# Optimization experiments

Hardware: AMD Instinct MI355X
Metric: run time of the kernel (lower is better)

Reference implementation:

```python
import jax, jax.numpy as jnp
import numpy as np

B, S, D, H = 4, 2048, 1024, 16
DH = D // H


def setup_inputs() -> dict:
    key = jax.random.key(0)
    ks = jax.random.split(key, 7)
    return {
        "Q": jax.random.normal(ks[0], (B, S, D), dtype=jnp.float32),
        "K": jax.random.normal(ks[1], (B, S, D), dtype=jnp.float32),
        "V": jax.random.normal(ks[2], (B, S, D), dtype=jnp.float32),
        "q_proj": jax.random.normal(ks[3], (D, D), dtype=jnp.float32),
        "k_proj": jax.random.normal(ks[4], (D, D), dtype=jnp.float32),
        "v_proj": jax.random.normal(ks[5], (D, D), dtype=jnp.float32),
        "output_proj": jax.random.normal(ks[6], (D, D), dtype=jnp.float32),
        "casual": 1,
    }


def reference(Q, K, V, q_proj, k_proj, v_proj, output_proj, casual):
    # projections: einsum('... a b, ... s b -> ... s a') == x @ W.T
    q = jnp.einsum('bsd,ad->bsa', Q, q_proj)
    k = jnp.einsum('bsd,ad->bsa', K, k_proj)
    v = jnp.einsum('bsd,ad->bsa', V, v_proj)
    # split heads: [B, S, H, DH]
    q = q.reshape(B, S, H, DH)
    k = k.reshape(B, S, H, DH)
    v = v.reshape(B, S, H, DH)
    # scores [B, H, Sq, Sk]
    scores = jnp.einsum('bqhd,bkhd->bhqk', q, k) / np.sqrt(DH).astype(np.float32)
    # causal mask: 0 on lower triangle, -inf above
    causal_mask = jnp.where(
        jnp.tril(jnp.ones((S, S), dtype=bool)), 0.0, -jnp.inf
    ).astype(scores.dtype)
    scores = scores + causal_mask
    attn = jax.nn.softmax(scores, axis=-1)
    # weighted values -> [B, Sq, H, DH] -> [B, Sq, D]
    out = jnp.einsum('bhqk,bkhd->bqhd', attn, v).reshape(B, S, D)
    # output projection: einsum('... a b, ... b -> ... a') == x @ W.T
    return jnp.einsum('bsd,ad->bsa', out, output_proj)
```

## Files before the change

kernel.cpp:

```cpp
#include <hip/hip_runtime.h>


typedef __attribute__((ext_vector_type(8))) _Float16 half8;
typedef __attribute__((ext_vector_type(4))) float f32x4;

#define DEVI static __device__ __forceinline__

static constexpr int cB = 4, cS = 2048, cD = 1024, cH = 16, cDH = 64;
static constexpr int cM = cB * cS;

DEVI unsigned short h2b(_Float16 h) { union { _Float16 f; unsigned short u; } x; x.f = h; return x.u; }

DEVI void async16(const void* g, void* l) {
#if defined(__HIP_DEVICE_COMPILE__)
  __builtin_amdgcn_global_load_lds((const __attribute__((address_space(1))) unsigned int*)g,
                                   (__attribute__((address_space(3))) unsigned int*)l, 16, 0, 0);
#endif
}

__global__ void split4_kernel(const float* __restrict__ Wq, const float* __restrict__ Wk,
                              const float* __restrict__ Wv, const float* __restrict__ Wo,
                              unsigned short* __restrict__ Wqh, unsigned short* __restrict__ Wql,
                              unsigned short* __restrict__ Wkh, unsigned short* __restrict__ Wkl,
                              unsigned short* __restrict__ Wvh, unsigned short* __restrict__ Woh) {
  const int w = blockIdx.x >> 10, blk = blockIdx.x & 1023;
  const float* in = (w == 0) ? Wq : (w == 1) ? Wk : (w == 2) ? Wv : Wo;
  unsigned short* hi = (w == 0) ? Wqh : (w == 1) ? Wkh : (w == 2) ? Wvh : Woh;
  unsigned short* lo = (w == 0) ? Wql : (w == 1) ? Wkl : nullptr;
  int i = (blk * 256 + (int)threadIdx.x) * 4;
  float4 v = *(const float4*)(in + i);
  _Float16 h0 = (_Float16)v.x, h1 = (_Float16)v.y, h2 = (_Float16)v.z, h3 = (_Float16)v.w;
  unsigned short th[4] = {h2b(h0), h2b(h1), h2b(h2), h2b(h3)};
  *(uint2*)(hi + i) = *(const uint2*)th;
  if (lo != nullptr) {
    unsigned short tl[4] = {h2b((_Float16)(v.x - (float)h0)), h2b((_Float16)(v.y - (float)h1)),
                            h2b((_Float16)(v.z - (float)h2)), h2b((_Float16)(v.w - (float)h3))};
    *(uint2*)(lo + i) = *(const uint2*)tl;
  }
}

__global__ __launch_bounds__(256, 3) void proj_fused(
    const float* __restrict__ Qa, const float* __restrict__ Ka, const float* __restrict__ Va,
    const unsigned short* __restrict__ Wqh, const unsigned short* __restrict__ Wql,
    const unsigned short* __restrict__ Wkh, const unsigned short* __restrict__ Wkl,
    const unsigned short* __restrict__ Wvh,
    unsigned short* __restrict__ qph, unsigned short* __restrict__ qpl,
    unsigned short* __restrict__ kph, unsigned short* __restrict__ kpl,
    unsigned short* __restrict__ vp) {
  constexpr int N = cD, K = cD;
  __shared__ float sA32[128 * 32];
  __shared__ unsigned short sBh[128 * 32];
  __shared__ unsigned short sBl[128 * 32];

  const int wid = (blockIdx.x & 7) * 192 + (blockIdx.x >> 3);
  const int job = wid >> 9;
  const int bid = wid & 511;
  const bool p3 = (job < 2);
  const float* A32p = (job == 0) ? Qa : (job == 1) ? Ka : Va;
  const unsigned short* Bh = (job == 0) ? Wqh : (job == 1) ? Wkh : Wvh;
  const unsigned short* Bl = (job == 0) ? Wql : Wkl;
  unsigned short* C0 = (job == 0) ? qph : (job == 1) ? kph : vp;
  unsigned short* C1 = (job == 0) ? qpl : kpl;

  const int tid = threadIdx.x, lane = tid & 63, wave = tid >> 6;
  const int wm = wave >> 1, wn = wave & 1;
  const int bm = bid >> 3, bn = bid & 7;
  const long r0 = (long)bm * 128, c0 = (long)bn * 128;
  const int quad = lane >> 4, cl = lane & 15;

  f32x4 acc[4][4];
#pragma unroll
  for (int mt = 0; mt < 4; ++mt)
#pragma unroll
    for (int nt = 0; nt < 4; ++nt) acc[mt][nt] = f32x4{0.f, 0.f, 0.f, 0.f};

  const int lrow8 = lane >> 3, lg8 = lane & 7;
  const int lrow16 = lane >> 2, lg4 = lane & 3;

  for (int k0 = 0; k0 < K; k0 += 32) {
    __syncthreads();
#pragma unroll
    for (int c = 0; c < 4; ++c) {
      int cc = wave * 4 + c;
      int r = cc * 8 + lrow8;
      const float* g = A32p + (r0 + r) * (long)K + k0 + ((lg8 ^ lrow8) * 4);
      async16(g, sA32 + cc * 256);
    }
#pragma unroll
    for (int c = 0; c < 2; ++c) {
      int cc = wave * 2 + c;
      int r = cc * 16 + lrow16;
      long gb = (c0 + r) * (long)K + k0 + ((lg4 ^ ((lrow16 >> 1) & 3)) * 8);
      async16(Bh + gb, sBh + cc * 512);
      if (p3) async16(Bl + gb, sBl + cc * 512);
    }
    __syncthreads();

    half8 ah[4], al[4], bh8[4], bl8[4];
#pragma unroll
    for (int mt = 0; mt < 4; ++mt) {
      int r = wm * 64 + mt * 16 + cl;
      int s0 = (quad * 2 + 0) ^ (r & 7), s1 = (quad * 2 + 1) ^ (r & 7);
      float fa[8];
      *(float4*)(fa) = *(const float4*)(sA32 + r * 32 + s0 * 4);
      *(float4*)(fa + 4) = *(const float4*)(sA32 + r * 32 + s1 * 4);
#pragma unroll
      for (int j = 0; j < 8; ++j) {
        _Float16 hh = (_Float16)fa[j];
        ah[mt][j] = hh;
        if (p3) al[mt][j] = (_Float16)(fa[j] - (float)hh);
      }
    }
#pragma unroll
    for (int nt = 0; nt < 4; ++nt) {
      int r = wn * 64 + nt * 16 + cl;
      int s = quad ^ ((r >> 1) & 3);
      bh8[nt] = *(const half8*)(sBh + r * 32 + s * 8);
      if (p3) bl8[nt] = *(const half8*)(sBl + r * 32 + s * 8);
    }
#pragma unroll
    for (int mt = 0; mt < 4; ++mt)
#pragma unroll
      for (int nt = 0; nt < 4; ++nt) {
        acc[mt][nt] = __builtin_amdgcn_mfma_f32_16x16x32_f16(ah[mt], bh8[nt], acc[mt][nt], 0, 0, 0);
        if (p3) {
          acc[mt][nt] = __builtin_amdgcn_mfma_f32_16x16x32_f16(ah[mt], bl8[nt], acc[mt][nt], 0, 0, 0);
          acc[mt][nt] = __builtin_amdgcn_mfma_f32_16x16x32_f16(al[mt], bh8[nt], acc[mt][nt], 0, 0, 0);
        }
      }
  }

#pragma unroll
  for (int mt = 0; mt < 4; ++mt)
#pragma unroll
    for (int nt = 0; nt < 4; ++nt)
#pragma unroll
      for (int i = 0; i < 4; ++i) {
        long row = r0 + wm * 64 + mt * 16 + quad * 4 + i;
        long col = c0 + wn * 64 + nt * 16 + cl;
        float v = acc[mt][nt][i];
        if (p3) {
          _Float16 hh = (_Float16)v;
          C0[row * N + col] = h2b(hh);
          C1[row * N + col] = h2b((_Float16)(v - (float)hh));
        } else {
          C0[row * N + col] = h2b((_Float16)v);
        }
      }
}

__global__ __launch_bounds__(256, 2) void gemm_out(const unsigned short* __restrict__ A16p,
                                                   const unsigned short* __restrict__ Bh,
                                                   float* __restrict__ C0, int M, int N, int K) {
  __shared__ unsigned short sA16[128 * 32];
  __shared__ unsigned short sBh[128 * 32];

  const int tid = threadIdx.x, lane = tid & 63, wave = tid >> 6;
  const int wm = wave >> 1, wn = wave & 1;
  const int nb = N >> 7;
  const int wid = ((int)blockIdx.x & 7) * 64 + ((int)blockIdx.x >> 3);
  const int bm = wid / nb, bn = wid % nb;
  const long r0 = (long)bm * 128, c0 = (long)bn * 128;
  const int quad = lane >> 4, cl = lane & 15;

  f32x4 acc[4][4];
#pragma unroll
  for (int mt = 0; mt < 4; ++mt)
#pragma unroll
    for (int nt = 0; nt < 4; ++nt) acc[mt][nt] = f32x4{0.f, 0.f, 0.f, 0.f};

  const int lrow16 = lane >> 2, lg4 = lane & 3;

  for (int k0 = 0; k0 < K; k0 += 32) {
    __syncthreads();
#pragma unroll
    for (int c = 0; c < 2; ++c) {
      int cc = wave * 2 + c;
      int r = cc * 16 + lrow16;
      long ga = (r0 + r) * (long)K + k0 + ((lg4 ^ ((lrow16 >> 1) & 3)) * 8);
      async16(A16p + ga, sA16 + cc * 512);
      long gb = (c0 + r) * (long)K + k0 + ((lg4 ^ ((lrow16 >> 1) & 3)) * 8);
      async16(Bh + gb, sBh + cc * 512);
    }
    __syncthreads();

    half8 ah[4], bh8[4];
#pragma unroll
    for (int mt = 0; mt < 4; ++mt) {
      int r = wm * 64 + mt * 16 + cl;
      int s = quad ^ ((r >> 1) & 3);
      ah[mt] = *(const half8*)(sA16 + r * 32 + s * 8);
    }
#pragma unroll
    for (int nt = 0; nt < 4; ++nt) {
      int r = wn * 64 + nt * 16 + cl;
      int s = quad ^ ((r >> 1) & 3);
      bh8[nt] = *(const half8*)(sBh + r * 32 + s * 8);
    }
#pragma unroll
    for (int mt = 0; mt < 4; ++mt)
#pragma unroll
      for (int nt = 0; nt < 4; ++nt)
        acc[mt][nt] = __builtin_amdgcn_mfma_f32_16x16x32_f16(ah[mt], bh8[nt], acc[mt][nt], 0, 0, 0);
  }

#pragma unroll
  for (int mt = 0; mt < 4; ++mt)
#pragma unroll
    for (int nt = 0; nt < 4; ++nt)
#pragma unroll
      for (int i = 0; i < 4; ++i) {
        long row = r0 + wm * 64 + mt * 16 + quad * 4 + i;
        long col = c0 + wn * 64 + nt * 16 + cl;
        C0[row * N + col] = acc[mt][nt][i];
      }
}

__global__ __launch_bounds__(256, 3) void flash_kernel(
    const unsigned short* __restrict__ qh_g, const unsigned short* __restrict__ ql_g,
    const unsigned short* __restrict__ kh_g, const unsigned short* __restrict__ kl_g,
    const unsigned short* __restrict__ vp_g, unsigned short* __restrict__ out) {
  __shared__ unsigned short sKh[64 * 64];
  __shared__ unsigned short sKl[64 * 64];
  __shared__ unsigned int sVtU[64 * 34];
  __shared__ unsigned short sP[4][32 * 40];

  const int tid = threadIdx.x, lane = tid & 63, wave = tid >> 6;
  const int quad = lane >> 4, cl = lane & 15;
  const int bh = blockIdx.x & 63;
  const int qt = 15 - (blockIdx.x >> 6);
  const int h = bh & 15;
  const int b = bh >> 4;
  const long rowbase = (long)b * cS;
  const int q0 = qt * 128;
  const int lrow8 = lane >> 3, lg8 = lane & 7;

  half8 qh[2][2], ql[2][2];
  const _Float16 s8 = (_Float16)0.125f;
#pragma unroll
  for (int ks = 0; ks < 2; ++ks)
#pragma unroll
    for (int mt = 0; mt < 2; ++mt) {
      long r = rowbase + q0 + wave * 32 + mt * 16 + cl;
      long off = r * cD + h * 64 + ks * 32 + quad * 8;
      qh[ks][mt] = *(const half8*)(qh_g + off) * s8;
      ql[ks][mt] = *(const half8*)(ql_g + off) * s8;
    }

  f32x4 O[2][5];
  float mrow[2][4];
#pragma unroll
  for (int mt = 0; mt < 2; ++mt) {
#pragma unroll
    for (int dt = 0; dt < 5; ++dt) O[mt][dt] = f32x4{0.f, 0.f, 0.f, 0.f};
#pragma unroll
    for (int i = 0; i < 4; ++i) mrow[mt][i] = -1e30f;
  }

  half8 vone;
#pragma unroll
  for (int j = 0; j < 8; ++j) vone[j] = (cl == 0) ? (_Float16)1.0f : (_Float16)0.0f;

  auto tile = [&](int ki, bool MASK) {
    __syncthreads();
#pragma unroll
    for (int c = 0; c < 2; ++c) {
      int cc = wave * 2 + c;
      int r = cc * 8 + lrow8;
      long g = (rowbase + ki * 64 + r) * (long)cD + h * 64 + ((lg8 ^ lrow8) * 8);
      async16(kh_g + g, sKh + cc * 512);
      async16(kl_g + g, sKl + cc * 512);
    }
    {
      int r2 = tid & 31, dc = (tid >> 5) * 8;
      const unsigned short* gv = vp_g + (rowbase + ki * 64 + 2 * r2) * (long)cD + h * 64 + dc;
      unsigned short a[8], bb[8];
      *(uint4*)a = *(const uint4*)gv;
      *(uint4*)bb = *(const uint4*)(gv + cD);
#pragma unroll
      for (int j = 0; j < 8; ++j)
        sVtU[(dc + j) * 34 + r2] = (unsigned int)a[j] | ((unsigned int)bb[j] << 16);
    }
    __syncthreads();

    f32x4 sacc[2][4];
#pragma unroll
    for (int mt = 0; mt < 2; ++mt)
#pragma unroll
      for (int nt = 0; nt < 4; ++nt) sacc[mt][nt] = f32x4{0.f, 0.f, 0.f, 0.f};
#pragma unroll
    for (int ks = 0; ks < 2; ++ks) {
      half8 kh8[4], kl8[4];
#pragma unroll
      for (int nt = 0; nt < 4; ++nt) {
        int r = nt * 16 + cl;
        int off = r * 64 + (((ks * 4 + quad) ^ (r & 7)) * 8);
        kh8[nt] = *(const half8*)(sKh + off);
        kl8[nt] = *(const half8*)(sKl + off);
      }
#pragma unroll
      for (int mt = 0; mt < 2; ++mt)
#pragma unroll
        for (int nt = 0; nt < 4; ++nt) {
          sacc[mt][nt] = __builtin_amdgcn_mfma_f32_16x16x32_f16(qh[ks][mt], kh8[nt], sacc[mt][nt], 0, 0, 0);
          sacc[mt][nt] = __builtin_amdgcn_mfma_f32_16x16x32_f16(qh[ks][mt], kl8[nt], sacc[mt][nt], 0, 0, 0);
          sacc[mt][nt] = __builtin_amdgcn_mfma_f32_16x16x32_f16(ql[ks][mt], kh8[nt], sacc[mt][nt], 0, 0, 0);
        }
    }
    if (MASK) {
#pragma unroll
      for (int mt = 0; mt < 2; ++mt)
#pragma unroll
        for (int nt = 0; nt < 4; ++nt)
#pragma unroll
          for (int i = 0; i < 4; ++i) {
            int rg = q0 + wave * 32 + mt * 16 + quad * 4 + i;
            int cg = ki * 64 + nt * 16 + cl;
            if (cg > rg) sacc[mt][nt][i] = -1e30f;
          }
    }
    float mnew[2][4];
    bool ch = false;
#pragma unroll
    for (int mt = 0; mt < 2; ++mt)
#pragma unroll
      for (int i = 0; i < 4; ++i) {
        float mx = fmaxf(fmaxf(sacc[mt][0][i], sacc[mt][1][i]),
                         fmaxf(sacc[mt][2][i], sacc[mt][3][i]));
#pragma unroll
        for (int d = 1; d < 16; d <<= 1) mx = fmaxf(mx, __shfl_xor(mx, d));
        ch |= (mx > mrow[mt][i]);
        mnew[mt][i] = fmaxf(mrow[mt][i], mx);
      }
    if (__ballot(ch)) {
#pragma unroll
      for (int mt = 0; mt < 2; ++mt)
#pragma unroll
        for (int i = 0; i < 4; ++i) {
          float a = __expf(mrow[mt][i] - mnew[mt][i]);
#pragma unroll
          for (int dt = 0; dt < 5; ++dt) O[mt][dt][i] *= a;
        }
    }
#pragma unroll
    for (int mt = 0; mt < 2; ++mt)
#pragma unroll
      for (int i = 0; i < 4; ++i) mrow[mt][i] = mnew[mt][i];

    unsigned short* sPw = sP[wave];
#pragma unroll
    for (int kc = 0; kc < 2; ++kc) {
#pragma unroll
      for (int mt = 0; mt < 2; ++mt)
#pragma unroll
        for (int ntl = 0; ntl < 2; ++ntl) {
          int nt = kc * 2 + ntl;
#pragma unroll
          for (int i = 0; i < 4; ++i) {
            float p = __expf(sacc[mt][nt][i] - mrow[mt][i]);
            sPw[(mt * 16 + quad * 4 + i) * 40 + ntl * 16 + cl] = h2b((_Float16)p);
          }
        }
      half8 pa[2], vb[4];
#pragma unroll
      for (int mt = 0; mt < 2; ++mt)
        pa[mt] = *(const half8*)(sPw + (mt * 16 + cl) * 40 + quad * 8);
#pragma unroll
      for (int dt = 0; dt < 4; ++dt) {
        int base = (dt * 16 + cl) * 34 + kc * 16 + quad * 4;
        union { uint4 u; half8 hh; } cvt;
        uint2 p0 = *(const uint2*)(sVtU + base);
        uint2 p1 = *(const uint2*)(sVtU + base + 2);
        cvt.u = uint4{p0.x, p0.y, p1.x, p1.y};
        vb[dt] = cvt.hh;
      }
#pragma unroll
      for (int mt = 0; mt < 2; ++mt) {
#pragma unroll
        for (int dt = 0; dt < 4; ++dt)
          O[mt][dt] = __builtin_amdgcn_mfma_f32_16x16x32_f16(pa[mt], vb[dt], O[mt][dt], 0, 0, 0);
        O[mt][4] = __builtin_amdgcn_mfma_f32_16x16x32_f16(pa[mt], vone, O[mt][4], 0, 0, 0);
      }
    }
  };

  const int full = 2 * qt;
  for (int ki = 0; ki < full; ++ki) tile(ki, false);
  tile(full, true);
  tile(full + 1, true);

  float lv[2][4];
#pragma unroll
  for (int mt = 0; mt < 2; ++mt)
#pragma unroll
    for (int i = 0; i < 4; ++i) lv[mt][i] = __shfl(O[mt][4][i], (lane & 48));
#pragma unroll
  for (int mt = 0; mt < 2; ++mt)
#pragma unroll
    for (int dt = 0; dt < 4; ++dt)
#pragma unroll
      for (int i = 0; i < 4; ++i) {
        long r = rowbase + q0 + wave * 32 + mt * 16 + quad * 4 + i;
        out[r * cD + h * 64 + dt * 16 + cl] = h2b((_Float16)(O[mt][dt][i] / lv[mt][i]));
      }
}

extern "C" void kernel_launch(void* const* d_in, const int* in_sizes, int n_in,
                              void* d_out, int out_size, void* d_ws, size_t ws_size,
                              hipStream_t stream) {
  const float* Q = (const float*)d_in[0];
  const float* K = (const float*)d_in[1];
  const float* V = (const float*)d_in[2];
  const float* Wq = (const float*)d_in[3];
  const float* Wk = (const float*)d_in[4];
  const float* Wv = (const float*)d_in[5];
  const float* Wo = (const float*)d_in[6];

  unsigned short* ws = (unsigned short*)d_ws;
  const size_t WD = (size_t)cD * cD;
  const size_t WM = (size_t)cM * cD;
  unsigned short* Wqh = ws;
  unsigned short* Wql = Wqh + WD;
  unsigned short* Wkh = Wql + WD;
  unsigned short* Wkl = Wkh + WD;
  unsigned short* Wvh = Wkl + WD;
  unsigned short* Woh = Wvh + WD;
  unsigned short* qph = Woh + WD;
  unsigned short* qpl = qph + WM;
  unsigned short* kph = qpl + WM;
  unsigned short* kpl = kph + WM;
  unsigned short* vp = kpl + WM;
  unsigned short* attnb = vp + WM;

  split4_kernel<<<4096, 256, 0, stream>>>(Wq, Wk, Wv, Wo, Wqh, Wql, Wkh, Wkl, Wvh, Woh);

  proj_fused<<<1536, 256, 0, stream>>>(Q, K, V, Wqh, Wql, Wkh, Wkl, Wvh,
                                       qph, qpl, kph, kpl, vp);

  flash_kernel<<<cB * cH * 16, 256, 0, stream>>>(qph, qpl, kph, kpl, vp, attnb);

  const int gblk = (cM / 128) * (cD / 128);
  gemm_out<<<gblk, 256, 0, stream>>>(attnb, Woh, (float*)d_out, cM, cD, cD);
}
```

Measured before the change: 544.5 us.

## Pre-split Q/K activations to fp16 pairs and double-buffer the projection GEMMs

Adds a separate kernel that splits the Q and K activations into fp16 hi/lo pairs ahead of time, so the Q/K projection GEMM loads fp16 tiles directly instead of converting fp32 in the inner loop. The fused projection is split into a Q/K kernel and a V kernel. All projection and output GEMMs get double-buffered LDS staging with a single barrier per k-step. Workspace is reused by aliasing the output buffer and intermediate regions, at the cost of an extra full pass over the activations and more LDS per block.

```diff
diff --git a/kernel.cpp b/kernel.cpp
--- a/kernel.cpp
+++ b/kernel.cpp
@@ -39,34 +39,53 @@
   }
 }
 
-__global__ __launch_bounds__(256, 3) void proj_fused(
-    const float* __restrict__ Qa, const float* __restrict__ Ka, const float* __restrict__ Va,
+__global__ void split_act_kernel(const float* __restrict__ Q, const float* __restrict__ K,
+                                 unsigned short* __restrict__ Qh, unsigned short* __restrict__ Ql,
+                                 unsigned short* __restrict__ Kh, unsigned short* __restrict__ Kl) {
+  const int t = blockIdx.x >> 13;
+  const int blk = blockIdx.x & 8191;
+  const float* in = t ? K : Q;
+  unsigned short* hi = t ? Kh : Qh;
+  unsigned short* lo = t ? Kl : Ql;
+  int i = (blk * 256 + (int)threadIdx.x) * 4;
+  float4 v = *(const float4*)(in + i);
+  _Float16 h0 = (_Float16)v.x, h1 = (_Float16)v.y, h2 = (_Float16)v.z, h3 = (_Float16)v.w;
+  unsigned short th[4] = {h2b(h0), h2b(h1), h2b(h2), h2b(h3)};
+  *(uint2*)(hi + i) = *(const uint2*)th;
+  unsigned short tl[4] = {h2b((_Float16)(v.x - (float)h0)), h2b((_Float16)(v.y - (float)h1)),
+                          h2b((_Float16)(v.z - (float)h2)), h2b((_Float16)(v.w - (float)h3))};
+  *(uint2*)(lo + i) = *(const uint2*)tl;
+}
+
+__global__ __launch_bounds__(256, 2) void proj_qk(
+    const unsigned short* __restrict__ Qh, const unsigned short* __restrict__ Ql,
+    const unsigned short* __restrict__ Kh, const unsigned short* __restrict__ Kl,
     const unsigned short* __restrict__ Wqh, const unsigned short* __restrict__ Wql,
     const unsigned short* __restrict__ Wkh, const unsigned short* __restrict__ Wkl,
-    const unsigned short* __restrict__ Wvh,
     unsigned short* __restrict__ qph, unsigned short* __restrict__ qpl,
-    unsigned short* __restrict__ kph, unsigned short* __restrict__ kpl,
-    unsigned short* __restrict__ vp) {
+    unsigned short* __restrict__ kph, unsigned short* __restrict__ kpl) {
   constexpr int N = cD, K = cD;
-  __shared__ float sA32[128 * 32];
-  __shared__ unsigned short sBh[128 * 32];
-  __shared__ unsigned short sBl[128 * 32];
-
-  const int wid = (blockIdx.x & 7) * 192 + (blockIdx.x >> 3);
+  __shared__ unsigned short sAh[2][128 * 32];
+  __shared__ unsigned short sAl[2][128 * 32];
+  __shared__ unsigned short sBh[2][128 * 32];
+  __shared__ unsigned short sBl[2][128 * 32];
+
+  const int wid = ((int)blockIdx.x & 7) * 128 + ((int)blockIdx.x >> 3);
   const int job = wid >> 9;
   const int bid = wid & 511;
-  const bool p3 = (job < 2);
-  const float* A32p = (job == 0) ? Qa : (job == 1) ? Ka : Va;
-  const unsigned short* Bh = (job == 0) ? Wqh : (job == 1) ? Wkh : Wvh;
-  const unsigned short* Bl = (job == 0) ? Wql : Wkl;
-  unsigned short* C0 = (job == 0) ? qph : (job == 1) ? kph : vp;
-  unsigned short* C1 = (job == 0) ? qpl : kpl;
+  const unsigned short* Ah_g = job ? Kh : Qh;
+  const unsigned short* Al_g = job ? Kl : Ql;
+  const unsigned short* Bh = job ? Wkh : Wqh;
+  const unsigned short* Bl = job ? Wkl : Wql;
+  unsigned short* C0 = job ? kph : qph;
+  unsigned short* C1 = job ? kpl : qpl;
 
   const int tid = threadIdx.x, lane = tid & 63, wave = tid >> 6;
   const int wm = wave >> 1, wn = wave & 1;
   const int bm = bid >> 3, bn = bid & 7;
   const long r0 = (long)bm * 128, c0 = (long)bn * 128;
   const int quad = lane >> 4, cl = lane & 15;
+  const int lrow16 = lane >> 2, lg4 = lane & 3;
 
   f32x4 acc[4][4];
 #pragma unroll
@@ -74,61 +93,148 @@
 #pragma unroll
     for (int nt = 0; nt < 4; ++nt) acc[mt][nt] = f32x4{0.f, 0.f, 0.f, 0.f};
 
+  auto stage = [&](int k0, int buf) {
+#pragma unroll
+    for (int c = 0; c < 2; ++c) {
+      int cc = wave * 2 + c;
+      int r = cc * 16 + lrow16;
+      int sw = (lg4 ^ ((lrow16 >> 1) & 3)) * 8;
+      long ga = (r0 + r) * (long)K + k0 + sw;
+      long gb = (c0 + r) * (long)K + k0 + sw;
+      async16(Ah_g + ga, &sAh[buf][cc * 512]);
+      async16(Al_g + ga, &sAl[buf][cc * 512]);
+      async16(Bh + gb, &sBh[buf][cc * 512]);
+      async16(Bl + gb, &sBl[buf][cc * 512]);
+    }
+  };
+
+  auto compute = [&](int buf) {
+    half8 ah[4], al[4], bh8[4], bl8[4];
+#pragma unroll
+    for (int mt = 0; mt < 4; ++mt) {
+      int r = wm * 64 + mt * 16 + cl;
+      int s = quad ^ ((r >> 1) & 3);
+      ah[mt] = *(const half8*)(&sAh[buf][r * 32 + s * 8]);
+      al[mt] = *(const half8*)(&sAl[buf][r * 32 + s * 8]);
+    }
+#pragma unroll
+    for (int nt = 0; nt < 4; ++nt) {
+      int r = wn * 64 + nt * 16 + cl;
+      int s = quad ^ ((r >> 1) & 3);
+      bh8[nt] = *(const half8*)(&sBh[buf][r * 32 + s * 8]);
+      bl8[nt] = *(const half8*)(&sBl[buf][r * 32 + s * 8]);
+    }
+#pragma unroll
+    for (int mt = 0; mt < 4; ++mt)
+#pragma unroll
+      for (int nt = 0; nt < 4; ++nt) {
+        acc[mt][nt] = __builtin_amdgcn_mfma_f32_16x16x32_f16(ah[mt], bh8[nt], acc[mt][nt], 0, 0, 0);
+        acc[mt][nt] = __builtin_amdgcn_mfma_f32_16x16x32_f16(ah[mt], bl8[nt], acc[mt][nt], 0, 0, 0);
+        acc[mt][nt] = __builtin_amdgcn_mfma_f32_16x16x32_f16(al[mt], bh8[nt], acc[mt][nt], 0, 0, 0);
+      }
+  };
+
+  stage(0, 0);
+  __syncthreads();
+  int cur = 0;
+  for (int k0 = 32; k0 < K; k0 += 32) {
+    stage(k0, cur ^ 1);
+    compute(cur);
+    __syncthreads();
+    cur ^= 1;
+  }
+  compute(cur);
+
+#pragma unroll
+  for (int mt = 0; mt < 4; ++mt)
+#pragma unroll
+    for (int nt = 0; nt < 4; ++nt)
+#pragma unroll
+      for (int i = 0; i < 4; ++i) {
+        long row = r0 + wm * 64 + mt * 16 + quad * 4 + i;
+        long col = c0 + wn * 64 + nt * 16 + cl;
+        float v = acc[mt][nt][i];
+        _Float16 hh = (_Float16)v;
+        C0[row * N + col] = h2b(hh);
+        C1[row * N + col] = h2b((_Float16)(v - (float)hh));
+      }
+}
+
+__global__ __launch_bounds__(256, 3) void proj_v(const float* __restrict__ Va,
+                                                 const unsigned short* __restrict__ Wvh,
+                                                 unsigned short* __restrict__ vp) {
+  constexpr int N = cD, K = cD;
+  __shared__ float sA32[2][128 * 32];
+  __shared__ unsigned short sBh[2][128 * 32];
+
+  const int wid = ((int)blockIdx.x & 7) * 64 + ((int)blockIdx.x >> 3);
+  const int bm = wid >> 3, bn = wid & 7;
+  const long r0 = (long)bm * 128, c0 = (long)bn * 128;
+
+  const int tid = threadIdx.x, lane = tid & 63, wave = tid >> 6;
+  const int wm = wave >> 1, wn = wave & 1;
+  const int quad = lane >> 4, cl = lane & 15;
   const int lrow8 = lane >> 3, lg8 = lane & 7;
   const int lrow16 = lane >> 2, lg4 = lane & 3;
 
-  for (int k0 = 0; k0 < K; k0 += 32) {
-    __syncthreads();
+  f32x4 acc[4][4];
+#pragma unroll
+  for (int mt = 0; mt < 4; ++mt)
+#pragma unroll
+    for (int nt = 0; nt < 4; ++nt) acc[mt][nt] = f32x4{0.f, 0.f, 0.f, 0.f};
+
+  auto stage = [&](int k0, int buf) {
 #pragma unroll
     for (int c = 0; c < 4; ++c) {
       int cc = wave * 4 + c;
       int r = cc * 8 + lrow8;
-      const float* g = A32p + (r0 + r) * (long)K + k0 + ((lg8 ^ lrow8) * 4);
-      async16(g, sA32 + cc * 256);
+      const float* g = Va + (r0 + r) * (long)K + k0 + ((lg8 ^ lrow8) * 4);
+      async16(g, &sA32[buf][cc * 256]);
     }
 #pragma unroll
     for (int c = 0; c < 2; ++c) {
       int cc = wave * 2 + c;
       int r = cc * 16 + lrow16;
       long gb = (c0 + r) * (long)K + k0 + ((lg4 ^ ((lrow16 >> 1) & 3)) * 8);
-      async16(Bh + gb, sBh + cc * 512);
-      if (p3) async16(Bl + gb, sBl + cc * 512);
-    }
-    __syncthreads();
-
-    half8 ah[4], al[4], bh8[4], bl8[4];
+      async16(Wvh + gb, &sBh[buf][cc * 512]);
+    }
+  };
+
+  auto compute = [&](int buf) {
+    half8 ah[4], bh8[4];
 #pragma unroll
     for (int mt = 0; mt < 4; ++mt) {
       int r = wm * 64 + mt * 16 + cl;
       int s0 = (quad * 2 + 0) ^ (r & 7), s1 = (quad * 2 + 1) ^ (r & 7);
       float fa[8];
-      *(float4*)(fa) = *(const float4*)(sA32 + r * 32 + s0 * 4);
-      *(float4*)(fa + 4) = *(const float4*)(sA32 + r * 32 + s1 * 4);
-#pragma unroll
-      for (int j = 0; j < 8; ++j) {
-        _Float16 hh = (_Float16)fa[j];
-        ah[mt][j] = hh;
-        if (p3) al[mt][j] = (_Float16)(fa[j] - (float)hh);
-      }
+      *(float4*)(fa) = *(const float4*)(&sA32[buf][r * 32 + s0 * 4]);
+      *(float4*)(fa + 4) = *(const float4*)(&sA32[buf][r * 32 + s1 * 4]);
+#pragma unroll
+      for (int j = 0; j < 8; ++j) ah[mt][j] = (_Float16)fa[j];
     }
 #pragma unroll
     for (int nt = 0; nt < 4; ++nt) {
       int r = wn * 64 + nt * 16 + cl;
       int s = quad ^ ((r >> 1) & 3);
-      bh8[nt] = *(const half8*)(sBh + r * 32 + s * 8);
-      if (p3) bl8[nt] = *(const half8*)(sBl + r * 32 + s * 8);
+      bh8[nt] = *(const half8*)(&sBh[buf][r * 32 + s * 8]);
     }
 #pragma unroll
     for (int mt = 0; mt < 4; ++mt)
 #pragma unroll
-      for (int nt = 0; nt < 4; ++nt) {
+      for (int nt = 0; nt < 4; ++nt)
         acc[mt][nt] = __builtin_amdgcn_mfma_f32_16x16x32_f16(ah[mt], bh8[nt], acc[mt][nt], 0, 0, 0);
-        if (p3) {
-          acc[mt][nt] = __builtin_amdgcn_mfma_f32_16x16x32_f16(ah[mt], bl8[nt], acc[mt][nt], 0, 0, 0);
-          acc[mt][nt] = __builtin_amdgcn_mfma_f32_16x16x32_f16(al[mt], bh8[nt], acc[mt][nt], 0, 0, 0);
-        }
-      }
+  };
+
+  stage(0, 0);
+  __syncthreads();
+  int cur = 0;
+  for (int k0 = 32; k0 < K; k0 += 32) {
+    stage(k0, cur ^ 1);
+    compute(cur);
+    __syncthreads();
+    cur ^= 1;
   }
+  compute(cur);
 
 #pragma unroll
   for (int mt = 0; mt < 4; ++mt)
@@ -138,22 +244,15 @@
       for (int i = 0; i < 4; ++i) {
         long row = r0 + wm * 64 + mt * 16 + quad * 4 + i;
         long col = c0 + wn * 64 + nt * 16 + cl;
-        float v = acc[mt][nt][i];
-        if (p3) {
-          _Float16 hh = (_Float16)v;
-          C0[row * N + col] = h2b(hh);
-          C1[row * N + col] = h2b((_Float16)(v - (float)hh));
-        } else {
-          C0[row * N + col] = h2b((_Float16)v);
-        }
-      }
-}
-
-__global__ __launch_bounds__(256, 2) void gemm_out(const unsigned short* __restrict__ A16p,
+        vp[row * N + col] = h2b((_Float16)acc[mt][nt][i]);
+      }
+}
+
+__global__ __launch_bounds__(256, 3) void gemm_out(const unsigned short* __restrict__ A16p,
                                                    const unsigned short* __restrict__ Bh,
                                                    float* __restrict__ C0, int M, int N, int K) {
-  __shared__ unsigned short sA16[128 * 32];
-  __shared__ unsigned short sBh[128 * 32];
+  __shared__ unsigned short sA16[2][128 * 32];
+  __shared__ unsigned short sB16[2][128 * 32];
 
   const int tid = threadIdx.x, lane = tid & 63, wave = tid >> 6;
   const int wm = wave >> 1, wn = wave & 1;
@@ -162,6 +261,7 @@
   const int bm = wid / nb, bn = wid % nb;
   const long r0 = (long)bm * 128, c0 = (long)bn * 128;
   const int quad = lane >> 4, cl = lane & 15;
+  const int lrow16 = lane >> 2, lg4 = lane & 3;
 
   f32x4 acc[4][4];
 #pragma unroll
@@ -169,40 +269,48 @@
 #pragma unroll
     for (int nt = 0; nt < 4; ++nt) acc[mt][nt] = f32x4{0.f, 0.f, 0.f, 0.f};
 
-  const int lrow16 = lane >> 2, lg4 = lane & 3;
-
-  for (int k0 = 0; k0 < K; k0 += 32) {
-    __syncthreads();
+  auto stage = [&](int k0, int buf) {
 #pragma unroll
     for (int c = 0; c < 2; ++c) {
       int cc = wave * 2 + c;
       int r = cc * 16 + lrow16;
-      long ga = (r0 + r) * (long)K + k0 + ((lg4 ^ ((lrow16 >> 1) & 3)) * 8);
-      async16(A16p + ga, sA16 + cc * 512);
-      long gb = (c0 + r) * (long)K + k0 + ((lg4 ^ ((lrow16 >> 1) & 3)) * 8);
-      async16(Bh + gb, sBh + cc * 512);
-    }
-    __syncthreads();
-
+      int sw = (lg4 ^ ((lrow16 >> 1) & 3)) * 8;
+      async16(A16p + (r0 + r) * (long)K + k0 + sw, &sA16[buf][cc * 512]);
+      async16(Bh + (c0 + r) * (long)K + k0 + sw, &sB16[buf][cc * 512]);
+    }
+  };
+
+  auto compute = [&](int buf) {
     half8 ah[4], bh8[4];
 #pragma unroll
     for (int mt = 0; mt < 4; ++mt) {
       int r = wm * 64 + mt * 16 + cl;
       int s = quad ^ ((r >> 1) & 3);
-      ah[mt] = *(const half8*)(sA16 + r * 32 + s * 8);
+      ah[mt] = *(const half8*)(&sA16[buf][r * 32 + s * 8]);
     }
 #pragma unroll
     for (int nt = 0; nt < 4; ++nt) {
       int r = wn * 64 + nt * 16 + cl;
       int s = quad ^ ((r >> 1) & 3);
-      bh8[nt] = *(const half8*)(sBh + r * 32 + s * 8);
+      bh8[nt] = *(const half8*)(&sB16[buf][r * 32 + s * 8]);
     }
 #pragma unroll
     for (int mt = 0; mt < 4; ++mt)
 #pragma unroll
       for (int nt = 0; nt < 4; ++nt)
         acc[mt][nt] = __builtin_amdgcn_mfma_f32_16x16x32_f16(ah[mt], bh8[nt], acc[mt][nt], 0, 0, 0);
+  };
+
+  stage(0, 0);
+  __syncthreads();
+  int cur = 0;
+  for (int k0 = 32; k0 < K; k0 += 32) {
+    stage(k0, cur ^ 1);
+    compute(cur);
+    __syncthreads();
+    cur ^= 1;
   }
+  compute(cur);
 
 #pragma unroll
   for (int mt = 0; mt < 4; ++mt)
@@ -425,17 +533,26 @@
   unsigned short* Wkl = Wkh + WD;
   unsigned short* Wvh = Wkl + WD;
   unsigned short* Woh = Wvh + WD;
-  unsigned short* qph = Woh + WD;
+  unsigned short* R1 = Woh + WD;
+  unsigned short* R2 = R1 + WM;
+  unsigned short* qph = R2 + WM;
   unsigned short* qpl = qph + WM;
   unsigned short* kph = qpl + WM;
   unsigned short* kpl = kph + WM;
-  unsigned short* vp = kpl + WM;
-  unsigned short* attnb = vp + WM;
+
+  unsigned short* Qh = (unsigned short*)d_out;
+  unsigned short* Ql = Qh + WM;
+  unsigned short* Kh = R1;
+  unsigned short* Kl = R2;
+  unsigned short* vp = R1;
+  unsigned short* attnb = R2;
 
   split4_kernel<<<4096, 256, 0, stream>>>(Wq, Wk, Wv, Wo, Wqh, Wql, Wkh, Wkl, Wvh, Woh);
-
-  proj_fused<<<1536, 256, 0, stream>>>(Q, K, V, Wqh, Wql, Wkh, Wkl, Wvh,
-                                       qph, qpl, kph, kpl, vp);
+  split_act_kernel<<<16384, 256, 0, stream>>>(Q, K, Qh, Ql, Kh, Kl);
+
+  proj_qk<<<1024, 256, 0, stream>>>(Qh, Ql, Kh, Kl, Wqh, Wql, Wkh, Wkl,
+                                    qph, qpl, kph, kpl);
+  proj_v<<<512, 256, 0, stream>>>(V, Wvh, vp);
 
   flash_kernel<<<cB * cH * 16, 256, 0, stream>>>(qph, qpl, kph, kpl, vp, attnb);
 
```

Result: faster. 509.1 us (-6.5%).
